# Performance work log

Measured on AMD Instinct MI355X. Metric: run time of the kernel, lower is better.

Reference implementation:

```python
import jax, jax.numpy as jnp
import numpy as np

DIM = 2048
HEADS = 16
HEAD_DIM = DIM // HEADS
B, S = 2, 2048


def setup_inputs() -> dict:
    key = jax.random.key(0)
    k1, k2, k3 = jax.random.split(key, 3)
    x = jax.random.normal(k1, (B, S, DIM), dtype=jnp.float32)
    # causal mask (True = keep), realistic production usage of masked_fill(mask==0,...)
    mask = jnp.tril(jnp.ones((S, S), dtype=bool))
    scale = 1.0 / np.sqrt(DIM)
    W_qkv = jax.random.normal(k2, (DIM, 3 * DIM), dtype=jnp.float32) * scale
    b_qkv = jnp.zeros((3 * DIM,), dtype=jnp.float32)
    W_out = jax.random.normal(k3, (DIM, DIM), dtype=jnp.float32) * scale
    b_out = jnp.zeros((DIM,), dtype=jnp.float32)
    return {"x": x, "mask": mask, "W_qkv": W_qkv, "b_qkv": b_qkv,
            "W_out": W_out, "b_out": b_out}


def reference(x, mask, W_qkv, b_qkv, W_out, b_out):
    b, s, d = x.shape
    # fused QKV projection: [b,s,3d]
    qkv = jnp.einsum('bsd,de->bse', x, W_qkv) + b_qkv
    # [b, s, h, 3*hd] -> [b, h, s, 3*hd] -> chunk into q,k,v
    qkv = qkv.reshape(b, s, HEADS, 3 * HEAD_DIM).transpose(0, 2, 1, 3)
    q, k, v = jnp.split(qkv, 3, axis=-1)  # each [b,h,s,hd]
    scores = jnp.einsum('bhqd,bhkd->bhqk', q, k) / np.sqrt(HEAD_DIM)
    scores = jnp.where(mask, scores, jnp.float32(-1e9))
    attn = jax.nn.softmax(scores, axis=-1)
    # dropout_rate = 0.0 (eval) -> identity
    out = jnp.einsum('bhqk,bhkd->bhqd', attn, v)  # [b,h,s,hd]
    out = out.transpose(0, 2, 1, 3).reshape(b, s, d)
    return jnp.einsum('bsd,de->bse', out, W_out) + b_out
```

## Files before the change

### kernel.cpp

```cpp
#include <hip/hip_runtime.h>
#include <hip/hip_bf16.h>

#define SEQ   2048
#define DIMSZ 2048
#define NHEAD 16
#define HD    128
#define KDIM  2048

typedef __attribute__((ext_vector_type(8))) short bf16x8;
typedef __attribute__((ext_vector_type(4))) float f32x4;
typedef __attribute__((ext_vector_type(4))) short short4v;
typedef __attribute__((ext_vector_type(4))) float float4v;

__device__ __forceinline__ short f2bf(float f) {
    union { __hip_bfloat16 h; short s; } u;
    u.h = __float2bfloat16(f);
    return u.s;
}

__device__ __forceinline__ unsigned pack_bf2(float lo, float hi) {
    return (unsigned)(unsigned short)f2bf(lo) | ((unsigned)(unsigned short)f2bf(hi) << 16);
}

__device__ __forceinline__ void gload_lds16(const void* g, void* l) {
    __builtin_amdgcn_global_load_lds(
        (const __attribute__((address_space(1))) void*)g,
        (__attribute__((address_space(3))) void*)l, 16, 0, 0);
}

__global__ __launch_bounds__(256) void cvt_bf16(const float* __restrict__ in,
                                                short* __restrict__ out) {
    int i = (blockIdx.x * 256 + threadIdx.x) * 4;
    float4v v = *reinterpret_cast<const float4v*>(in + i);
    short4v o;
    o[0] = f2bf(v[0]); o[1] = f2bf(v[1]); o[2] = f2bf(v[2]); o[3] = f2bf(v[3]);
    *reinterpret_cast<short4v*>(out + i) = o;
}

__global__ __launch_bounds__(256) void transpose_cvt(const float* __restrict__ in,
                                                     short* __restrict__ out,
                                                     int R, int C) {
    __shared__ float tile[32][33];
    int c0 = blockIdx.x * 32, r0 = blockIdx.y * 32;
    int tx = threadIdx.x, ty = threadIdx.y;
#pragma unroll
    for (int i = 0; i < 32; i += 8)
        tile[ty + i][tx] = in[(long)(r0 + ty + i) * C + c0 + tx];
    __syncthreads();
#pragma unroll
    for (int i = 0; i < 32; i += 8)
        out[(long)(c0 + ty + i) * R + r0 + tx] = f2bf(tile[tx][ty + i]);
}

template <int MODE, int BM, int BN, int WMC, int WNC>
__global__ __launch_bounds__(512, 2) void gemm8p(const short* __restrict__ A,
                                                 const short* __restrict__ Bt,
                                                 const float* __restrict__ bias,
                                                 float* __restrict__ outf,
                                                 short* __restrict__ q_buf,
                                                 short* __restrict__ k_buf,
                                                 short* __restrict__ vt_buf,
                                                 int ntx) {
    constexpr int QMW = (BM / 2) / WMC;
    constexpr int QNW = (BN / 2) / WNC;
    constexpr int MA = QMW / 16;
    constexpr int NB = QNW / 16;
    constexpr int UA = BM / 64, UB = BN / 64, UT = UA + UB;
    constexpr int RA = MA * 2, RB = NB * 2;
    constexpr int BH0C = (BN / 2 + 63) / 64;
    constexpr int NE = UA / 2 + BH0C, NL = UT - NE;
    constexpr int S0 = 2, S2 = 2;
    constexpr int VM0 = NE + S0;
    constexpr int VM2 = NL + S2;
    constexpr int VM3 = (NE - S2) + NE;
    constexpr int NT = KDIM / 64;

    __shared__ __align__(16) short Alds[2][BM * 64];
    __shared__ __align__(16) short Blds[2][BN * 64];

    const int tid = threadIdx.x;
    const int wv = tid >> 6, ln = tid & 63;
    const int lr = ln & 15, lg = ln >> 4;
    const int wm = wv / WNC, wn = wv % WNC;
    const int q8 = gridDim.x >> 3;
    const int id = blockIdx.x;
    const int swz = (id & 7) * q8 + (id >> 3);
    const int m0 = (swz / ntx) * BM, n0 = (swz % ntx) * BN;

    const int r_l = wv * 8 + (ln >> 3);
    const int g8 = ((ln & 7) ^ ((ln >> 3) & 7)) << 3;

#define STAGE_U(u, bufi, TT)                                                   \
    {                                                                          \
        const bool isA_ = (u) < UA / 2 || (u) >= UA / 2 + UB;                  \
        const int idx_ = (u) < UA / 2 ? (u)                                    \
                         : ((u) < UA / 2 + UB ? (u) - UA / 2 : (u) - UB);      \
        if (isA_)                                                              \
            gload_lds16(A + (long)(m0 + idx_ * 64 + r_l) * KDIM + (TT)*64 + g8,\
                        &Alds[bufi][idx_ * 4096 + wv * 512]);                  \
        else                                                                   \
            gload_lds16(Bt + (long)(n0 + idx_ * 64 + r_l) * KDIM + (TT)*64 + g8,\
                        &Blds[bufi][idx_ * 4096 + wv * 512]);                  \
    }

#define RD(L_, row_, kk_) \
    (*reinterpret_cast<const bf16x8*>(&(L_)[(row_)*64 + ((((kk_)*4 + lg) ^ ((row_)&7)) << 3)]))

#define RD_A(bufi, mh, bank)                                                   \
    _Pragma("unroll") for (int mi = 0; mi < MA; ++mi) {                        \
        int r_ = (mh) * (BM / 2) + wm * QMW + mi * 16 + lr;                    \
        bank[mi][0] = RD(Alds[bufi], r_, 0);                                   \
        bank[mi][1] = RD(Alds[bufi], r_, 1);                                   \
    }
#define RD_B(bufi, nh, bank)                                                   \
    _Pragma("unroll") for (int ni = 0; ni < NB; ++ni) {                        \
        int r_ = (nh) * (BN / 2) + wn * QNW + ni * 16 + lr;                    \
        bank[ni][0] = RD(Blds[bufi], r_, 0);                                   \
        bank[ni][1] = RD(Blds[bufi], r_, 1);                                   \
    }

#define MFMA_Q(qi, AB, BB)                                                     \
    __builtin_amdgcn_s_setprio(1);                                             \
    _Pragma("unroll") for (int kk = 0; kk < 2; ++kk)                           \
        _Pragma("unroll") for (int mi = 0; mi < MA; ++mi)                      \
            _Pragma("unroll") for (int ni = 0; ni < NB; ++ni)                  \
                acc[qi][mi][ni] = __builtin_amdgcn_mfma_f32_16x16x32_bf16(     \
                    AB[mi][kk], BB[ni][kk], acc[qi][mi][ni], 0, 0, 0);         \
    __builtin_amdgcn_s_setprio(0);

#define LGKM(n)                                                                \
    asm volatile("s_waitcnt lgkmcnt(%0)" ::"i"(n) : "memory");                 \
    __builtin_amdgcn_sched_barrier(0);
#define VMC(n) asm volatile("s_waitcnt vmcnt(%0)" ::"i"(n) : "memory");
#define BAR()                                                                  \
    __builtin_amdgcn_s_barrier();                                              \
    __builtin_amdgcn_sched_barrier(0);

    f32x4 acc[4][MA][NB] = {};
    bf16x8 aF0[MA][2], aF1[MA][2], bF0a[NB][2], bF0b[NB][2], bF1[NB][2];

#pragma unroll
    for (int u = 0; u < UT; ++u) STAGE_U(u, 0, 0);
#pragma unroll
    for (int u = 0; u < NE; ++u) STAGE_U(u, 1, 1);
    VMC(NE);
    BAR();
    RD_A(0, 0, aF0);
    RD_B(0, 0, bF0a);

#define TILE_BODY(PAR, T_, BF0C, BF0N)                                         \
    {                                                                          \
        constexpr int cur = PAR, nxt = PAR ^ 1;                                \
        RD_B(cur, 1, bF1);                                                     \
        if ((T_) + 1 < NT) {                                                   \
            STAGE_U(NE + 0, nxt, (T_) + 1);                                    \
            STAGE_U(NE + 1, nxt, (T_) + 1);                                    \
        }                                                                      \
        LGKM(RB);                                                              \
        MFMA_Q(0, aF0, BF0C);                                                  \
        VMC(VM0);                                                              \
        BAR();                                                                 \
        RD_A(cur, 1, aF1);                                                     \
        if ((T_) + 1 < NT) {                                                   \
            _Pragma("unroll") for (int u = NE + S0; u < UT; ++u)               \
                STAGE_U(u, nxt, (T_) + 1);                                     \
        }                                                                      \
        LGKM(RA);                                                              \
        MFMA_Q(1, aF0, bF1);                                                   \
        BAR();                                                                 \
        if ((T_) + 2 < NT) {                                                   \
            STAGE_U(0, cur, (T_) + 2);                                         \
            STAGE_U(1, cur, (T_) + 2);                                         \
        }                                                                      \
        LGKM(0);                                                               \
        MFMA_Q(2, aF1, bF1);                                                   \
        if ((T_) + 2 < NT) { VMC(VM2); } else { VMC(NL); }                     \
        BAR();                                                                 \
        if ((T_) + 1 < NT) {                                                   \
            RD_A(nxt, 0, aF0);                                                 \
            RD_B(nxt, 0, BF0N);                                                \
        }                                                                      \
        if ((T_) + 2 < NT) {                                                   \
            _Pragma("unroll") for (int u = S2; u < NE; ++u)                    \
                STAGE_U(u, cur, (T_) + 2);                                     \
        }                                                                      \
        LGKM(RA + RB);                                                         \
        MFMA_Q(3, aF1, BF0C);                                                  \
        if ((T_) + 2 < NT) { VMC(VM3); } else { VMC(0); }                      \
        BAR();                                                                 \
    }

    for (int TT = 0; TT < NT; TT += 2) {
        TILE_BODY(0, TT, bF0a, bF0b);
        TILE_BODY(1, TT + 1, bF0b, bF0a);
    }

    const int MH[4] = {0, 0, 1, 1}, NHq[4] = {0, 1, 1, 0};
#pragma unroll
    for (int q = 0; q < 4; ++q) {
#pragma unroll
        for (int mi = 0; mi < MA; ++mi) {
#pragma unroll
            for (int ni = 0; ni < NB; ++ni) {
                int col = n0 + NHq[q] * (BN / 2) + wn * QNW + ni * 16 + lr;
                float bv = bias[col];
#pragma unroll
                for (int j = 0; j < 4; ++j) {
                    int row = m0 + MH[q] * (BM / 2) + wm * QMW + mi * 16 + lg * 4 + j;
                    float v = acc[q][mi][ni][j] + bv;
                    if (MODE == 0) {
                        int h = col / (3 * HD);
                        int jj = col - h * (3 * HD);
                        int b = row >> 11, s = row & 2047;
                        int bh = b * NHEAD + h;
                        short sv = f2bf(v);
                        if (jj < HD)
                            q_buf[(bh * SEQ + s) * HD + jj] = sv;
                        else if (jj < 2 * HD)
                            k_buf[(bh * SEQ + s) * HD + (jj - HD)] = sv;
                        else
                            vt_buf[(bh * HD + (jj - 2 * HD)) * SEQ + s] = sv;
                    } else {
                        outf[(long)row * DIMSZ + col] = v;
                    }
                }
            }
        }
    }
#undef STAGE_U
#undef RD
#undef RD_A
#undef RD_B
#undef MFMA_Q
#undef LGKM
#undef VMC
#undef BAR
#undef TILE_BODY
}

__global__ __launch_bounds__(256, 2) void attn_kernel(const short* __restrict__ q_buf,
                                                      const short* __restrict__ k_buf,
                                                      const short* __restrict__ vt_buf,
                                                      short* __restrict__ ao) {
    __shared__ __align__(16) short Klds[2][64 * 128];
    __shared__ __align__(16) short Vlds[2][128 * 64];
    const int tid = threadIdx.x;
    const int wave = tid >> 6, lane = tid & 63;
    const int lr = lane & 15, lg = lane >> 4;
    const int bx = blockIdx.x;
    const int qt = 15 - (bx >> 5);
    const int bh = bx & 31;
    const int b = bh >> 4, h = bh & 15;
    const int qbase = qt * 128 + wave * 32;
    const float c2 = 0.12752775f;

    bf16x8 qf[2][4];
    {
        const short* qrow = q_buf + ((long)(bh * SEQ + qbase + lr)) * HD;
#pragma unroll
        for (int mi = 0; mi < 2; ++mi)
#pragma unroll
            for (int c = 0; c < 4; ++c)
                qf[mi][c] = *reinterpret_cast<const bf16x8*>(
                    qrow + mi * 16 * HD + c * 32 + lg * 8);
    }
    asm volatile("s_waitcnt vmcnt(0)" ::: "memory");

    const char* kbase = (const char*)(k_buf + (long)bh * SEQ * HD);
    const char* vbase = (const char*)(vt_buf + (long)bh * HD * SEQ);
    const int krow_l = wave * 4 + (lane >> 4);
    const int kcol_l = ((lane & 15) * 16) ^ ((krow_l & 7) << 4);
    const int vrow_l = wave * 8 + (lane >> 3);
    const int vcol_l = ((lane & 7) * 16) ^ ((vrow_l & 7) << 4);

    const int nt = 2 * (qt + 1);
    auto stage = [&](int bufi, int t) {
        const char* ks = kbase + (long)t * 16384 + (long)krow_l * 256 + kcol_l;
        const char* vs = vbase + (long)t * 128 + (long)vrow_l * (SEQ * 2) + vcol_l;
        short* kd = &Klds[bufi][wave * 512];
        short* vd = &Vlds[bufi][wave * 512];
#pragma unroll
        for (int i = 0; i < 4; ++i) {
            gload_lds16(ks + i * 4096, kd + i * 2048);
            gload_lds16(vs + (long)i * 32 * SEQ * 2, vd + i * 2048);
        }
    };

    f32x4 o_acc[2][8] = {};
    float mrow[2] = {-1e30f, -1e30f}, lrow[2] = {0.f, 0.f};

    const int s0 = (lane & 15) | ((lane & 16) << 1);
    const int s1 = s0 + 16;
    const bool hi_ni = (lane & 32) != 0;

    stage(0, 0);
    for (int t = 0; t < nt; ++t) {
        const int cur = t & 1;
        if (t + 1 < nt) {
            stage(cur ^ 1, t + 1);
            asm volatile("s_waitcnt vmcnt(8)" ::: "memory");
        } else {
            asm volatile("s_waitcnt vmcnt(0)" ::: "memory");
        }
        __builtin_amdgcn_s_barrier();
        __builtin_amdgcn_sched_barrier(0);

        const int kv0 = t * 64;
        if (kv0 <= qbase + 31) {
            f32x4 sc[2][4] = {};
            const short* kl = &Klds[cur][0];
#pragma unroll
            for (int c = 0; c < 4; ++c) {
                bf16x8 kf[4];
#pragma unroll
                for (int ni = 0; ni < 4; ++ni)
                    kf[ni] = *reinterpret_cast<const bf16x8*>(
                        kl + (((ni * 16 + lr) * 256 +
                               ((c * 64 + lg * 16) ^ ((lr & 7) << 4))) >> 1));
                __builtin_amdgcn_s_setprio(1);
#pragma unroll
                for (int mi = 0; mi < 2; ++mi)
#pragma unroll
                    for (int ni = 0; ni < 4; ++ni)
                        sc[mi][ni] = __builtin_amdgcn_mfma_f32_16x16x32_bf16(
                            kf[ni], qf[mi][c], sc[mi][ni], 0, 0, 0);
                __builtin_amdgcn_s_setprio(0);
            }
            const bool full = (kv0 + 63) <= qbase;
            float pv[2][4][4], mx[2];
#pragma unroll
            for (int mi = 0; mi < 2; ++mi) {
                float m_ = -3e38f;
                const int qg = qbase + mi * 16 + lr;
#pragma unroll
                for (int ni = 0; ni < 4; ++ni)
#pragma unroll
                    for (int j = 0; j < 4; ++j) {
                        float v = sc[mi][ni][j] * c2;
                        if (!full && (kv0 + ni * 16 + lg * 4 + j > qg)) v = -1e9f;
                        pv[mi][ni][j] = v;
                        m_ = fmaxf(m_, v);
                    }
                mx[mi] = m_;
            }
#pragma unroll
            for (int mi = 0; mi < 2; ++mi) {
                mx[mi] = fmaxf(mx[mi], __shfl_xor(mx[mi], 16, 64));
                mx[mi] = fmaxf(mx[mi], __shfl_xor(mx[mi], 32, 64));
            }
            float md = fmaxf(mx[0] - mrow[0], mx[1] - mrow[1]);
            if (!__all(md <= 11.5f)) {
#pragma unroll
                for (int mi = 0; mi < 2; ++mi) {
                    float mn = fmaxf(mrow[mi], mx[mi]);
                    float a = exp2f(mrow[mi] - mn);
                    mrow[mi] = mn;
                    lrow[mi] *= a;
#pragma unroll
                    for (int j = 0; j < 4; ++j) {
                        float aj = __shfl(a, (lane & 48) | (lg * 4 + j), 64);
#pragma unroll
                        for (int n = 0; n < 8; ++n)
                            o_acc[mi][n][j] *= aj;
                    }
                }
            }
            unsigned pk[2][4][2];
#pragma unroll
            for (int mi = 0; mi < 2; ++mi) {
                float ps = 0.f;
#pragma unroll
                for (int ni = 0; ni < 4; ++ni) {
#pragma unroll
                    for (int j = 0; j < 4; ++j) {
                        float p = exp2f(pv[mi][ni][j] - mrow[mi]);
                        pv[mi][ni][j] = p;
                        ps += p;
                    }
                    pk[mi][ni][0] = pack_bf2(pv[mi][ni][0], pv[mi][ni][1]);
                    pk[mi][ni][1] = pack_bf2(pv[mi][ni][2], pv[mi][ni][3]);
                }
                ps += __shfl_xor(ps, 16, 64);
                ps += __shfl_xor(ps, 32, 64);
                lrow[mi] += ps;
            }
            const short* vl = &Vlds[cur][0];
#pragma unroll
            for (int kc = 0; kc < 2; ++kc) {
                union { int i[4]; bf16x8 v; } pa[2];
#pragma unroll
                for (int mi = 0; mi < 2; ++mi) {
                    int a0 = __shfl((int)pk[mi][2 * kc][0], s0, 64);
                    int b0 = __shfl((int)pk[mi][2 * kc + 1][0], s0, 64);
                    int a1 = __shfl((int)pk[mi][2 * kc][1], s0, 64);
                    int b1 = __shfl((int)pk[mi][2 * kc + 1][1], s0, 64);
                    int a2 = __shfl((int)pk[mi][2 * kc][0], s1, 64);
                    int b2 = __shfl((int)pk[mi][2 * kc + 1][0], s1, 64);
                    int a3 = __shfl((int)pk[mi][2 * kc][1], s1, 64);
                    int b3 = __shfl((int)pk[mi][2 * kc + 1][1], s1, 64);
                    pa[mi].i[0] = hi_ni ? b0 : a0;
                    pa[mi].i[1] = hi_ni ? b1 : a1;
                    pa[mi].i[2] = hi_ni ? b2 : a2;
                    pa[mi].i[3] = hi_ni ? b3 : a3;
                }
#pragma unroll
                for (int n = 0; n < 8; ++n) {
                    bf16x8 vf = *reinterpret_cast<const bf16x8*>(
                        vl + (((n * 16 + lr) * 128 +
                               ((kc * 64 + lg * 16) ^ ((lr & 7) << 4))) >> 1));
                    __builtin_amdgcn_s_setprio(1);
#pragma unroll
                    for (int mi = 0; mi < 2; ++mi)
                        o_acc[mi][n] = __builtin_amdgcn_mfma_f32_16x16x32_bf16(
                            pa[mi].v, vf, o_acc[mi][n], 0, 0, 0);
                    __builtin_amdgcn_s_setprio(0);
                }
            }
        }
        __builtin_amdgcn_s_barrier();
    }

    float invq[2];
#pragma unroll
    for (int mi = 0; mi < 2; ++mi) invq[mi] = 1.0f / lrow[mi];
    short* aor = ao + ((long)(b * SEQ + qbase) * DIMSZ + h * HD);
#pragma unroll
    for (int mi = 0; mi < 2; ++mi)
#pragma unroll
        for (int j = 0; j < 4; ++j) {
            float ij = __shfl(invq[mi], (lane & 48) | (lg * 4 + j), 64);
#pragma unroll
            for (int n = 0; n < 8; ++n)
                aor[(mi * 16 + lg * 4 + j) * DIMSZ + n * 16 + lr] =
                    f2bf(o_acc[mi][n][j] * ij);
        }
}

extern "C" void kernel_launch(void* const* d_in, const int* in_sizes, int n_in,
                              void* d_out, int out_size, void* d_ws, size_t ws_size,
                              hipStream_t stream) {
    const float* x     = (const float*)d_in[0];
    const float* W_qkv = (const float*)d_in[2];
    const float* b_qkv = (const float*)d_in[3];
    const float* W_out = (const float*)d_in[4];
    const float* b_out = (const float*)d_in[5];
    float* out = (float*)d_out;

    char* ws = (char*)d_ws;
    short* x_bf   = (short*)ws;
    short* wqkv_t = (short*)(ws + (size_t)16 * 1048576);
    short* wout_t = (short*)(ws + (size_t)40 * 1048576);
    short* q_buf  = (short*)(ws + (size_t)48 * 1048576);
    short* k_buf  = (short*)(ws + (size_t)64 * 1048576);
    short* vt_buf = (short*)(ws + (size_t)80 * 1048576);
    short* ao     = x_bf;

    cvt_bf16<<<8192, 256, 0, stream>>>(x, x_bf);
    transpose_cvt<<<dim3(192, 64), dim3(32, 8), 0, stream>>>(W_qkv, wqkv_t, 2048, 6144);
    transpose_cvt<<<dim3(64, 64), dim3(32, 8), 0, stream>>>(W_out, wout_t, 2048, 2048);
    gemm8p<0, 256, 192, 4, 2><<<512, 512, 0, stream>>>(x_bf, wqkv_t, b_qkv, nullptr,
                                                       q_buf, k_buf, vt_buf, 32);
    attn_kernel<<<512, 256, 0, stream>>>(q_buf, k_buf, vt_buf, ao);
    gemm8p<1, 128, 256, 2, 4><<<256, 512, 0, stream>>>(ao, wout_t, b_out, out,
                                                       nullptr, nullptr, nullptr, 8);
}
```

Measured before the change: 299.8 us.

## Simplify GEMM main loop to per-quadrant full waits and extra barriers

Replaces the software-pipelined GEMM loop, which prefetched the next tile's first A/B fragments and used partial lgkmcnt/vmcnt waits, with a simpler schedule. Each quadrant now reads its fragments from LDS, hits a barrier, waits for all LDS reads, and only then issues its MFMAs. This drops one fragment register bank and the cross-iteration prefetch, probably to cut register pressure or to fix a hazard. In exchange it adds more barriers and serialises LDS reads with the MFMAs, so less latency is hidden.

```diff
diff --git a/kernel.cpp b/kernel.cpp
--- a/kernel.cpp
+++ b/kernel.cpp
@@ -66,13 +66,9 @@
     constexpr int MA = QMW / 16;
     constexpr int NB = QNW / 16;
     constexpr int UA = BM / 64, UB = BN / 64, UT = UA + UB;
-    constexpr int RA = MA * 2, RB = NB * 2;
     constexpr int BH0C = (BN / 2 + 63) / 64;
     constexpr int NE = UA / 2 + BH0C, NL = UT - NE;
     constexpr int S0 = 2, S2 = 2;
-    constexpr int VM0 = NE + S0;
-    constexpr int VM2 = NL + S2;
-    constexpr int VM3 = (NE - S2) + NE;
     constexpr int NT = KDIM / 64;
 
     __shared__ __align__(16) short Alds[2][BM * 64];
@@ -128,8 +124,8 @@
                     AB[mi][kk], BB[ni][kk], acc[qi][mi][ni], 0, 0, 0);         \
     __builtin_amdgcn_s_setprio(0);
 
-#define LGKM(n)                                                                \
-    asm volatile("s_waitcnt lgkmcnt(%0)" ::"i"(n) : "memory");                 \
+#define LGKM0()                                                                \
+    asm volatile("s_waitcnt lgkmcnt(0)" ::: "memory");                         \
     __builtin_amdgcn_sched_barrier(0);
 #define VMC(n) asm volatile("s_waitcnt vmcnt(%0)" ::"i"(n) : "memory");
 #define BAR()                                                                  \
@@ -137,7 +133,7 @@
     __builtin_amdgcn_sched_barrier(0);
 
     f32x4 acc[4][MA][NB] = {};
-    bf16x8 aF0[MA][2], aF1[MA][2], bF0a[NB][2], bF0b[NB][2], bF1[NB][2];
+    bf16x8 aF0[MA][2], aF1[MA][2], bF0[NB][2], bF1[NB][2];
 
 #pragma unroll
     for (int u = 0; u < UT; ++u) STAGE_U(u, 0, 0);
@@ -145,54 +141,54 @@
     for (int u = 0; u < NE; ++u) STAGE_U(u, 1, 1);
     VMC(NE);
     BAR();
-    RD_A(0, 0, aF0);
-    RD_B(0, 0, bF0a);
-
-#define TILE_BODY(PAR, T_, BF0C, BF0N)                                         \
+
+#define TILE_BODY(PAR, T_)                                                     \
     {                                                                          \
         constexpr int cur = PAR, nxt = PAR ^ 1;                                \
-        RD_B(cur, 1, bF1);                                                     \
+                                      \
+        RD_A(cur, 0, aF0);                                                     \
+        RD_B(cur, 0, bF0);                                                     \
         if ((T_) + 1 < NT) {                                                   \
             STAGE_U(NE + 0, nxt, (T_) + 1);                                    \
             STAGE_U(NE + 1, nxt, (T_) + 1);                                    \
         }                                                                      \
-        LGKM(RB);                                                              \
-        MFMA_Q(0, aF0, BF0C);                                                  \
-        VMC(VM0);                                                              \
-        BAR();                                                                 \
-        RD_A(cur, 1, aF1);                                                     \
+        BAR();                                                                 \
+        LGKM0();                                                               \
+        MFMA_Q(0, aF0, bF0);                                                   \
+        BAR();                                                                 \
+                                        \
+        RD_B(cur, 1, bF1);                                                     \
         if ((T_) + 1 < NT) {                                                   \
             _Pragma("unroll") for (int u = NE + S0; u < UT; ++u)               \
                 STAGE_U(u, nxt, (T_) + 1);                                     \
         }                                                                      \
-        LGKM(RA);                                                              \
+        BAR();                                                                 \
+        LGKM0();                                                               \
         MFMA_Q(1, aF0, bF1);                                                   \
         BAR();                                                                 \
+                                \
+        RD_A(cur, 1, aF1);                                                     \
         if ((T_) + 2 < NT) {                                                   \
             STAGE_U(0, cur, (T_) + 2);                                         \
             STAGE_U(1, cur, (T_) + 2);                                         \
         }                                                                      \
-        LGKM(0);                                                               \
+        BAR();                                                                 \
+        LGKM0();                                                               \
         MFMA_Q(2, aF1, bF1);                                                   \
-        if ((T_) + 2 < NT) { VMC(VM2); } else { VMC(NL); }                     \
-        BAR();                                                                 \
-        if ((T_) + 1 < NT) {                                                   \
-            RD_A(nxt, 0, aF0);                                                 \
-            RD_B(nxt, 0, BF0N);                                                \
-        }                                                                      \
+        BAR();                                                                 \
+          \
         if ((T_) + 2 < NT) {                                                   \
             _Pragma("unroll") for (int u = S2; u < NE; ++u)                    \
                 STAGE_U(u, cur, (T_) + 2);                                     \
         }                                                                      \
-        LGKM(RA + RB);                                                         \
-        MFMA_Q(3, aF1, BF0C);                                                  \
-        if ((T_) + 2 < NT) { VMC(VM3); } else { VMC(0); }                      \
+        MFMA_Q(3, aF1, bF0);                                                   \
+        if ((T_) + 2 < NT) { VMC(NE); } else { VMC(0); }                       \
         BAR();                                                                 \
     }
 
     for (int TT = 0; TT < NT; TT += 2) {
-        TILE_BODY(0, TT, bF0a, bF0b);
-        TILE_BODY(1, TT + 1, bF0b, bF0a);
+        TILE_BODY(0, TT);
+        TILE_BODY(1, TT + 1);
     }
 
     const int MH[4] = {0, 0, 1, 1}, NHq[4] = {0, 1, 1, 0};
@@ -232,7 +228,7 @@
 #undef RD_A
 #undef RD_B
 #undef MFMA_Q
-#undef LGKM
+#undef LGKM0
 #undef VMC
 #undef BAR
 #undef TILE_BODY
```

Result: no change. 298.2 us (-0.5%).
